# Kernel tuning notes

Hardware: AMD Instinct MI355X
Metric: run time of the kernel (lower is better)

Reference implementation:

```python
import jax, jax.numpy as jnp
import numpy as np

EPSILON = 0.001
CAP = 2000.0
H, W, C, B = 224, 224, 1024, 256


def setup_inputs() -> dict:
    key = jax.random.key(0)
    k1, k2, k3, k4 = jax.random.split(key, 4)
    x = jax.random.normal(k1, (B, H, W), dtype=jnp.float32)
    positions = 0.5 + 0.3 * jax.random.normal(k2, (1, 1, C, 2), dtype=jnp.float32)
    sigmas = 0.02 * jax.random.normal(k3, (1, 1, C), dtype=jnp.float32)
    curve_weights = 0.2 * jax.random.normal(k4, (1, 1, C), dtype=jnp.float32)
    y_axis = jnp.linspace(0.0, 1.0, H + 1)[:-1]
    x_axis = jnp.linspace(0.0, 1.0, W + 1)[:-1]
    ys, xs = jnp.meshgrid(y_axis, x_axis, indexing='ij')
    return {"x": x, "positions": positions, "sigmas": sigmas,
            "curve_weights": curve_weights, "xs": xs.astype(jnp.float32),
            "ys": ys.astype(jnp.float32)}


def calc_curves(positions, sigmas, curve_weights, xs, ys):
    # sigmas/curve_weights: (1,1,C); xs/ys: (H,W)
    two_sig2 = 2.0 * sigmas ** 2 + EPSILON            # (1,1,C)
    factor = 1.0 / (2.0 * jnp.pi * sigmas ** 2 + EPSILON)
    grid = (xs[:, :, None] - positions[..., 1]) ** 2 + \
           (ys[:, :, None] - positions[..., 0]) ** 2   # (H,W,C)
    curves = factor * jnp.exp(-grid / two_sig2) * curve_weights
    return jnp.clip(curves, -CAP, CAP)                 # (H,W,C)


def reference(x, positions, sigmas, curve_weights, xs, ys):
    x = x.reshape(-1, H, W)
    curves = calc_curves(positions, sigmas, curve_weights, xs, ys)
    num_pixels = float(H * W)
    # sum over H,W of curves[None] * x[...,None]  ==  GEMM contraction
    out = jnp.einsum('bhw,hwc->bc', x, curves) / num_pixels
    return out
```

## Files before the change

### kernel.cpp

```cpp
#include <hip/hip_runtime.h>
#include <hip/hip_bf16.h>
#include <stdint.h>

#define HH 224
#define WW 224
#define CC 1024
#define BB 256
#define KK (HH*WW)
#define EPSILON_F 0.001f
#define LOG2E 1.4426950408889634f
#define INVN (1.0f/50176.0f)
#define CLAMP_V (2000.0f/50176.0f)

#define KCHUNKS 32
#define ROWS_PER_CHUNK 7
#define STEPS 49

#define LDS_STRIDE 36

typedef __bf16 bf16x8 __attribute__((ext_vector_type(8)));
typedef float  f32x4  __attribute__((ext_vector_type(4)));

__global__ __launch_bounds__(256)
void reduce_kernel(const float* __restrict__ part, float* __restrict__ out) {
    int i = blockIdx.x * 256 + threadIdx.x;
    f32x4 s = ((const f32x4*)out)[i];
#pragma unroll
    for (int z = 0; z < KCHUNKS - 1; ++z)
        s += ((const f32x4*)part)[(size_t)z * (BB * CC / 4) + i];
    ((f32x4*)out)[i] = s;
}

template <bool PARTIAL>
__global__ __launch_bounds__(256)
void blob_gemm_kernel(const float* __restrict__ x,
                      const float* __restrict__ pos,
                      const float* __restrict__ sig,
                      const float* __restrict__ cwt,
                      const float* __restrict__ xs,
                      const float* __restrict__ ys,
                      float* __restrict__ out,
                      float* __restrict__ part) {
    __shared__ __bf16 Bs[2][64 * LDS_STRIDE];
    __shared__ float  xrow[WW];
    __shared__ float  ycol[ROWS_PER_CHUNK];

    const int tid  = threadIdx.x;
    const int wave = tid >> 6;
    const int lane = tid & 63;

    const int id   = blockIdx.x;
    const int xcd  = id & 7;
    const int slot = id >> 3;
    const int z    = xcd * 4 + (slot & 3);
    const int cx   = slot >> 2;
    const int c0   = cx * 64;
    const int k0   = z * (ROWS_PER_CHUNK * WW);

    if (tid < WW) xrow[tid] = xs[tid];
    if (tid >= WW && tid < WW + ROWS_PER_CHUNK)
        ycol[tid - WW] = ys[(z * ROWS_PER_CHUNK + (tid - WW)) * WW];

    const int q   = tid & 3;
    const int cr0 = tid >> 2;
    const int c   = c0 + cr0;
    float A2, S2, P0, P1;
    {
        float s  = sig[c];
        float w  = cwt[c];
        float s2 = s * s;
        A2 = w / (6.283185307179586f * s2 + EPSILON_F) * INVN;
        S2 = LOG2E / (2.0f * s2 + EPSILON_F);
        P0 = pos[2 * c];
        P1 = pos[2 * c + 1];
    }
    const int bs_w = cr0 * LDS_STRIDE + q * 8;

    const int fl = lane & 15;
    const int fk = (lane >> 4) * 8;
    const int wm = wave * 64;
    const float* aff = x + (size_t)(wm + fl) * KK + k0 + fk;
    const int br_off = fl * LDS_STRIDE + fk;

    auto cvt_frag = [](float4 f0, float4 f1) -> bf16x8 {
        union { __bf16 h[8]; bf16x8 v; } t;
        t.h[0] = (__bf16)f0.x; t.h[1] = (__bf16)f0.y;
        t.h[2] = (__bf16)f0.z; t.h[3] = (__bf16)f0.w;
        t.h[4] = (__bf16)f1.x; t.h[5] = (__bf16)f1.y;
        t.h[6] = (__bf16)f1.z; t.h[7] = (__bf16)f1.w;
        return t.v;
    };

    f32x4 acc[4][4];
#pragma unroll
    for (int i = 0; i < 4; ++i)
#pragma unroll
        for (int j = 0; j < 4; ++j) acc[i][j] = (f32x4){0.f, 0.f, 0.f, 0.f};

    __syncthreads();

    float ycolr[ROWS_PER_CHUNK];
#pragma unroll
    for (int r = 0; r < ROWS_PER_CHUNK; ++r) ycolr[r] = ycol[r];

    float Ex[8];
    {
        float4 xv0 = *(const float4*)(xrow + q * 8);
        float4 xv1 = *(const float4*)(xrow + q * 8 + 4);
        float xv[8] = {xv0.x, xv0.y, xv0.z, xv0.w, xv1.x, xv1.y, xv1.z, xv1.w};
#pragma unroll
        for (int i = 0; i < 8; ++i) {
            float dx = xv[i] - P1;
            Ex[i] = __builtin_amdgcn_exp2f(-(dx * S2 * dx));
        }
        float dy  = ycolr[0] - P0;
        float eyA = __builtin_amdgcn_exp2f(-(dy * S2 * dy)) * A2;
        union { __bf16 h[8]; uint4 u; } cv;
#pragma unroll
        for (int i = 0; i < 8; ++i) {
            float v = Ex[i] * eyA;
            cv.h[i] = (__bf16)fminf(fmaxf(v, -CLAMP_V), CLAMP_V);
        }
        *(uint4*)(&Bs[0][bs_w]) = cv.u;
    }
    bf16x8 fa[4];
#pragma unroll
    for (int mi = 0; mi < 4; ++mi) {
        const float* p = aff + (size_t)mi * 16 * KK;
        fa[mi] = cvt_frag(*(const float4*)p, *(const float4*)(p + 4));
    }
    __syncthreads();

    int nr = 1, nwb = 0;
#pragma unroll 2
    for (int s = 0; s < STEPS; ++s) {
        const int cb = s & 1;

        float4 pf0[4], pf1[4];
        if (s < STEPS - 1) {
            const int koff = nr * WW + nwb * 32;
#pragma unroll
            for (int mi = 0; mi < 4; ++mi) {
                const float* p = aff + (size_t)mi * 16 * KK + koff;
                pf0[mi] = *(const float4*)(p);
                pf1[mi] = *(const float4*)(p + 4);
            }
        }

        bf16x8 fb[4];
#pragma unroll
        for (int ni = 0; ni < 4; ++ni)
            fb[ni] = *(const bf16x8*)(&Bs[cb][br_off + ni * 16 * LDS_STRIDE]);
#pragma unroll
        for (int mi = 0; mi < 4; ++mi)
#pragma unroll
            for (int ni = 0; ni < 4; ++ni)
                acc[mi][ni] = __builtin_amdgcn_mfma_f32_16x16x32_bf16(
                    fa[mi], fb[ni], acc[mi][ni], 0, 0, 0);

        if (s < STEPS - 1) {
            if (nr == 0) {
                float4 xv0 = *(const float4*)(xrow + nwb * 32 + q * 8);
                float4 xv1 = *(const float4*)(xrow + nwb * 32 + q * 8 + 4);
                float xv[8] = {xv0.x, xv0.y, xv0.z, xv0.w, xv1.x, xv1.y, xv1.z, xv1.w};
#pragma unroll
                for (int i = 0; i < 8; ++i) {
                    float dx = xv[i] - P1;
                    Ex[i] = __builtin_amdgcn_exp2f(-(dx * S2 * dx));
                }
            }
            float dy  = ycolr[nr] - P0;
            float eyA = __builtin_amdgcn_exp2f(-(dy * S2 * dy)) * A2;
            union { __bf16 h[8]; uint4 u; } cv;
#pragma unroll
            for (int i = 0; i < 8; ++i) {
                float v = Ex[i] * eyA;
                cv.h[i] = (__bf16)fminf(fmaxf(v, -CLAMP_V), CLAMP_V);
            }
            *(uint4*)(&Bs[cb ^ 1][bs_w]) = cv.u;
            ++nr;
            if (nr == ROWS_PER_CHUNK) { nr = 0; ++nwb; }
        }
        __syncthreads();
        if (s < STEPS - 1) {
#pragma unroll
            for (int mi = 0; mi < 4; ++mi) fa[mi] = cvt_frag(pf0[mi], pf1[mi]);
        }
    }

    const int orow = (lane >> 4) * 4;
    float* base;
    if (PARTIAL) base = (z == 0) ? out : (part + (size_t)(z - 1) * BB * CC);
    else         base = out;
#pragma unroll
    for (int mi = 0; mi < 4; ++mi) {
        int m = wm + mi * 16 + orow;
#pragma unroll
        for (int ni = 0; ni < 4; ++ni) {
            int cc = c0 + ni * 16 + fl;
#pragma unroll
            for (int v = 0; v < 4; ++v) {
                if (PARTIAL)
                    base[(size_t)(m + v) * CC + cc] = acc[mi][ni][v];
                else
                    atomicAdd(base + (size_t)(m + v) * CC + cc, acc[mi][ni][v]);
            }
        }
    }
}

extern "C" void kernel_launch(void* const* d_in, const int* in_sizes, int n_in,
                              void* d_out, int out_size, void* d_ws, size_t ws_size,
                              hipStream_t stream) {
    const float* x   = (const float*)d_in[0];
    const float* pos = (const float*)d_in[1];
    const float* sg  = (const float*)d_in[2];
    const float* cw  = (const float*)d_in[3];
    const float* xs  = (const float*)d_in[4];
    const float* ys  = (const float*)d_in[5];
    float* out = (float*)d_out;

    const int nblk = 16 * KCHUNKS;
    const size_t PSZ = (size_t)(KCHUNKS - 1) * BB * CC * 4;

    if (ws_size >= PSZ) {
        float* part = (float*)d_ws;
        blob_gemm_kernel<true><<<nblk, 256, 0, stream>>>(x, pos, sg, cw, xs, ys, out, part);
        reduce_kernel<<<BB * CC / 4 / 256, 256, 0, stream>>>(part, out);
    } else {
        hipMemsetAsync(out, 0, (size_t)BB * CC * sizeof(float), stream);
        blob_gemm_kernel<false><<<nblk, 256, 0, stream>>>(x, pos, sg, cw, xs, ys, out, nullptr);
    }
}
```

Measured before the change: 180.8 us.

## Generate curve B-fragments in registers per wave, removing LDS staging and barriers

Each lane now computes its own B fragment (the Gaussian curve values for its 4 column groups and 8 k values) directly in registers instead of writing a shared LDS tile that all waves read after a __syncthreads. This removes the per-step block barrier and LDS round trip, and the loop is restructured into a width-block by row nest with the row loop fully unrolled. Clamping now uses a med3 instruction. In exchange, each wave redundantly computes the curve values: four times the exp and convert work plus more registers (ExA[4][8], per-column parameters), which may raise VALU pressure and lower occupancy.

```diff
diff --git a/kernel.cpp b/kernel.cpp
--- a/kernel.cpp
+++ b/kernel.cpp
@@ -14,9 +14,7 @@
 
 #define KCHUNKS 32
 #define ROWS_PER_CHUNK 7
-#define STEPS 49
-
-#define LDS_STRIDE 36
+#define WBS 7
 
 typedef __bf16 bf16x8 __attribute__((ext_vector_type(8)));
 typedef float  f32x4  __attribute__((ext_vector_type(4)));
@@ -41,9 +39,8 @@
                       const float* __restrict__ ys,
                       float* __restrict__ out,
                       float* __restrict__ part) {
-    __shared__ __bf16 Bs[2][64 * LDS_STRIDE];
-    __shared__ float  xrow[WW];
-    __shared__ float  ycol[ROWS_PER_CHUNK];
+    __shared__ float xrow[WW];
+    __shared__ float ycol[ROWS_PER_CHUNK];
 
     const int tid  = threadIdx.x;
     const int wave = tid >> 6;
@@ -60,27 +57,45 @@
     if (tid < WW) xrow[tid] = xs[tid];
     if (tid >= WW && tid < WW + ROWS_PER_CHUNK)
         ycol[tid - WW] = ys[(z * ROWS_PER_CHUNK + (tid - WW)) * WW];
-
-    const int q   = tid & 3;
-    const int cr0 = tid >> 2;
-    const int c   = c0 + cr0;
-    float A2, S2, P0, P1;
-    {
+    __syncthreads();
+
+    const int fl = lane & 15;
+    const int fk = (lane >> 4) * 8;
+    const int wm = wave * 64;
+
+    float A2[4], S2[4], P0[4], P1[4];
+#pragma unroll
+    for (int ni = 0; ni < 4; ++ni) {
+        int c = c0 + ni * 16 + fl;
         float s  = sig[c];
         float w  = cwt[c];
         float s2 = s * s;
-        A2 = w / (6.283185307179586f * s2 + EPSILON_F) * INVN;
-        S2 = LOG2E / (2.0f * s2 + EPSILON_F);
-        P0 = pos[2 * c];
-        P1 = pos[2 * c + 1];
-    }
-    const int bs_w = cr0 * LDS_STRIDE + q * 8;
-
-    const int fl = lane & 15;
-    const int fk = (lane >> 4) * 8;
-    const int wm = wave * 64;
+        A2[ni] = w / (6.283185307179586f * s2 + EPSILON_F) * INVN;
+        S2[ni] = LOG2E / (2.0f * s2 + EPSILON_F);
+        P0[ni] = pos[2 * c];
+        P1[ni] = pos[2 * c + 1];
+    }
+
+    float ycolr[ROWS_PER_CHUNK];
+#pragma unroll
+    for (int r = 0; r < ROWS_PER_CHUNK; ++r) ycolr[r] = ycol[r];
+
     const float* aff = x + (size_t)(wm + fl) * KK + k0 + fk;
-    const int br_off = fl * LDS_STRIDE + fk;
+
+    float ExA[4][8];
+    auto refresh_ex = [&](int wb) {
+        float4 xa = *(const float4*)(xrow + wb * 32 + fk);
+        float4 xb = *(const float4*)(xrow + wb * 32 + fk + 4);
+        float xv[8] = {xa.x, xa.y, xa.z, xa.w, xb.x, xb.y, xb.z, xb.w};
+#pragma unroll
+        for (int ni = 0; ni < 4; ++ni)
+#pragma unroll
+            for (int j = 0; j < 8; ++j) {
+                float dx = xv[j] - P1[ni];
+                ExA[ni][j] = __builtin_amdgcn_exp2f(-(dx * S2[ni] * dx)) * A2[ni];
+            }
+    };
+    refresh_ex(0);
 
     auto cvt_frag = [](float4 f0, float4 f1) -> bf16x8 {
         union { __bf16 h[8]; bf16x8 v; } t;
@@ -97,94 +112,61 @@
 #pragma unroll
         for (int j = 0; j < 4; ++j) acc[i][j] = (f32x4){0.f, 0.f, 0.f, 0.f};
 
-    __syncthreads();
-
-    float ycolr[ROWS_PER_CHUNK];
-#pragma unroll
-    for (int r = 0; r < ROWS_PER_CHUNK; ++r) ycolr[r] = ycol[r];
-
-    float Ex[8];
-    {
-        float4 xv0 = *(const float4*)(xrow + q * 8);
-        float4 xv1 = *(const float4*)(xrow + q * 8 + 4);
-        float xv[8] = {xv0.x, xv0.y, xv0.z, xv0.w, xv1.x, xv1.y, xv1.z, xv1.w};
-#pragma unroll
-        for (int i = 0; i < 8; ++i) {
-            float dx = xv[i] - P1;
-            Ex[i] = __builtin_amdgcn_exp2f(-(dx * S2 * dx));
-        }
-        float dy  = ycolr[0] - P0;
-        float eyA = __builtin_amdgcn_exp2f(-(dy * S2 * dy)) * A2;
-        union { __bf16 h[8]; uint4 u; } cv;
-#pragma unroll
-        for (int i = 0; i < 8; ++i) {
-            float v = Ex[i] * eyA;
-            cv.h[i] = (__bf16)fminf(fmaxf(v, -CLAMP_V), CLAMP_V);
-        }
-        *(uint4*)(&Bs[0][bs_w]) = cv.u;
-    }
-    bf16x8 fa[4];
+    float4 pf0[4], pf1[4];
 #pragma unroll
     for (int mi = 0; mi < 4; ++mi) {
         const float* p = aff + (size_t)mi * 16 * KK;
-        fa[mi] = cvt_frag(*(const float4*)p, *(const float4*)(p + 4));
-    }
-    __syncthreads();
-
-    int nr = 1, nwb = 0;
-#pragma unroll 2
-    for (int s = 0; s < STEPS; ++s) {
-        const int cb = s & 1;
-
-        float4 pf0[4], pf1[4];
-        if (s < STEPS - 1) {
-            const int koff = nr * WW + nwb * 32;
-#pragma unroll
-            for (int mi = 0; mi < 4; ++mi) {
-                const float* p = aff + (size_t)mi * 16 * KK + koff;
-                pf0[mi] = *(const float4*)(p);
-                pf1[mi] = *(const float4*)(p + 4);
-            }
-        }
-
-        bf16x8 fb[4];
-#pragma unroll
-        for (int ni = 0; ni < 4; ++ni)
-            fb[ni] = *(const bf16x8*)(&Bs[cb][br_off + ni * 16 * LDS_STRIDE]);
-#pragma unroll
-        for (int mi = 0; mi < 4; ++mi)
-#pragma unroll
-            for (int ni = 0; ni < 4; ++ni)
-                acc[mi][ni] = __builtin_amdgcn_mfma_f32_16x16x32_bf16(
-                    fa[mi], fb[ni], acc[mi][ni], 0, 0, 0);
-
-        if (s < STEPS - 1) {
-            if (nr == 0) {
-                float4 xv0 = *(const float4*)(xrow + nwb * 32 + q * 8);
-                float4 xv1 = *(const float4*)(xrow + nwb * 32 + q * 8 + 4);
-                float xv[8] = {xv0.x, xv0.y, xv0.z, xv0.w, xv1.x, xv1.y, xv1.z, xv1.w};
-#pragma unroll
-                for (int i = 0; i < 8; ++i) {
-                    float dx = xv[i] - P1;
-                    Ex[i] = __builtin_amdgcn_exp2f(-(dx * S2 * dx));
+        pf0[mi] = *(const float4*)(p);
+        pf1[mi] = *(const float4*)(p + 4);
+    }
+    bf16x8 fa[4];
+#pragma unroll
+    for (int mi = 0; mi < 4; ++mi) fa[mi] = cvt_frag(pf0[mi], pf1[mi]);
+
+#pragma unroll 1
+    for (int wb = 0; wb < WBS; ++wb) {
+#pragma unroll
+        for (int r = 0; r < ROWS_PER_CHUNK; ++r) {
+            const bool last = (wb == WBS - 1) && (r == ROWS_PER_CHUNK - 1);
+
+            if (!last) {
+                int nr = r + 1, nwb = wb;
+                if (nr == ROWS_PER_CHUNK) { nr = 0; ++nwb; }
+                const int koff = nr * WW + nwb * 32;
+#pragma unroll
+                for (int mi = 0; mi < 4; ++mi) {
+                    const float* p = aff + (size_t)mi * 16 * KK + koff;
+                    pf0[mi] = *(const float4*)(p);
+                    pf1[mi] = *(const float4*)(p + 4);
                 }
             }
-            float dy  = ycolr[nr] - P0;
-            float eyA = __builtin_amdgcn_exp2f(-(dy * S2 * dy)) * A2;
-            union { __bf16 h[8]; uint4 u; } cv;
-#pragma unroll
-            for (int i = 0; i < 8; ++i) {
-                float v = Ex[i] * eyA;
-                cv.h[i] = (__bf16)fminf(fmaxf(v, -CLAMP_V), CLAMP_V);
-            }
-            *(uint4*)(&Bs[cb ^ 1][bs_w]) = cv.u;
-            ++nr;
-            if (nr == ROWS_PER_CHUNK) { nr = 0; ++nwb; }
-        }
-        __syncthreads();
-        if (s < STEPS - 1) {
-#pragma unroll
-            for (int mi = 0; mi < 4; ++mi) fa[mi] = cvt_frag(pf0[mi], pf1[mi]);
+
+            bf16x8 fb[4];
+#pragma unroll
+            for (int ni = 0; ni < 4; ++ni) {
+                float dy = ycolr[r] - P0[ni];
+                float ey = __builtin_amdgcn_exp2f(-(dy * S2[ni] * dy));
+                union { __bf16 h[8]; bf16x8 v; } t;
+#pragma unroll
+                for (int j = 0; j < 8; ++j) {
+                    float v = ExA[ni][j] * ey;
+                    t.h[j] = (__bf16)__builtin_amdgcn_fmed3f(v, -CLAMP_V, CLAMP_V);
+                }
+                fb[ni] = t.v;
+            }
+
+#pragma unroll
+            for (int mi = 0; mi < 4; ++mi)
+#pragma unroll
+                for (int ni = 0; ni < 4; ++ni)
+                    acc[mi][ni] = __builtin_amdgcn_mfma_f32_16x16x32_bf16(
+                        fa[mi], fb[ni], acc[mi][ni], 0, 0, 0);
+
+            if (!last) {
+#pragma unroll
+                for (int mi = 0; mi < 4; ++mi) fa[mi] = cvt_frag(pf0[mi], pf1[mi]);
+                if (r == ROWS_PER_CHUNK - 1) refresh_ex(wb + 1);
+            }
         }
     }
 
```

Measured after the change: 229.0 us. +26.6%, slower.
